# Performance work log

Hardware: AMD Instinct MI355X
Metric: run time of the kernel (lower is better)

The kernel has to match this reference:

```python
import jax, jax.numpy as jnp
import numpy as np

BG_W = 1.0
DILATED_BG_W = 5.0
EDGE_W = 20.0
KSIZE = 3


def setup_inputs() -> dict:
    key = jax.random.key(0)
    k1, k2 = jax.random.split(key)
    B, C, H, W = 16, 1, 1024, 1024
    pred = jax.random.normal(k1, (B, C, H, W), dtype=jnp.float32)
    target = (jax.random.uniform(k2, (B, C, H, W)) < 0.05).astype(jnp.float32)
    return {"pred": pred, "target": target}


def _dilate(target):
    # cv2.dilate with KSIZExKSIZE rect kernel == max pool, stride 1, SAME padding
    return jax.lax.reduce_window(
        target, -jnp.inf, jax.lax.max,
        window_dimensions=(1, 1, KSIZE, KSIZE),
        window_strides=(1, 1, 1, 1),
        padding="SAME",
    )


def reference(pred, target):
    dilated = _dilate(target)
    # weight: edge pixels (target>0.5) -> EDGE_W, else dilated band -> DILATED_BG_W, else BG_W
    weight = jnp.where(target > 0.5, EDGE_W,
                       jnp.where(dilated > 0.5, DILATED_BG_W, BG_W))
    # binary_cross_entropy_with_logits, reduction='none', then mean
    x = pred
    losses = weight * (jnp.maximum(x, 0.0) - x * target + jnp.log1p(jnp.exp(-jnp.abs(x))))
    return jnp.mean(losses)
```

## Files before the change

### kernel.cpp

```cpp
#include <hip/hip_runtime.h>

#define HH 1024
#define WW 1024
#define RPB 4
#define NT 1024

__device__ __forceinline__ float fmax3(float a, float b, float c) {
    return fmaxf(a, fmaxf(b, c));
}

__device__ __forceinline__ float loss_elem(float x, float t, float dil) {
    float w = fmaf(15.0f, t, fmaf(4.0f, dil, 1.0f));
    float a  = fabsf(x);
    float sp = __logf(1.0f + __expf(-a));
    return w * (fmaxf(x, 0.0f) - x * t + sp);
}

template <bool PER_WAVE>
__global__ __launch_bounds__(NT) void dilatedweightBCE_main(
        const float* __restrict__ pred,
        const float* __restrict__ target,
        float* __restrict__ partial) {
    __shared__ float swave[NT / 64];

    const int t    = threadIdx.x;
    const int lane = t & 63;
    const int w16  = t >> 6;
    const int rin  = t >> 8;
    const int c    = (t & 255) * 4;
    const int b    = blockIdx.y;
    const int h    = blockIdx.x * RPB + rin;

    const float* timg = target + (size_t)b * HH * WW;
    const size_t rowoff = (size_t)h * WW;
    const bool has_up = (h > 0);
    const bool has_dn = (h < HH - 1);
    const float4 zero = make_float4(0.0f, 0.0f, 0.0f, 0.0f);

    float4 tmid = *(const float4*)(timg + rowoff + c);
    float4 tup  = has_up ? *(const float4*)(timg + rowoff - WW + c) : zero;
    float4 tdn  = has_dn ? *(const float4*)(timg + rowoff + WW + c) : zero;
    float4 x    = *(const float4*)(pred + (size_t)b * HH * WW + rowoff + c);

    float halo = 0.0f;
    if (lane == 0 || lane == 63) {
        const int pc = (lane == 0) ? c - 1 : c + 4;
        if (pc >= 0 && pc < WW) {
            float v = timg[rowoff + pc];
            if (has_up) v = fmaxf(v, timg[rowoff - WW + pc]);
            if (has_dn) v = fmaxf(v, timg[rowoff + WW + pc]);
            halo = v;
        }
    }

    float4 vm = make_float4(fmax3(tup.x, tmid.x, tdn.x),
                            fmax3(tup.y, tmid.y, tdn.y),
                            fmax3(tup.z, tmid.z, tdn.z),
                            fmax3(tup.w, tmid.w, tdn.w));

    float l  = __shfl_up(vm.w, 1);
    float rr = __shfl_down(vm.x, 1);
    if (lane == 0)  l  = halo;
    if (lane == 63) rr = halo;

    float d0 = fmax3(l,    vm.x, vm.y);
    float d1 = fmax3(vm.x, vm.y, vm.z);
    float d2 = fmax3(vm.y, vm.z, vm.w);
    float d3 = fmax3(vm.z, vm.w, rr);

    float s = 0.0f;
    s += loss_elem(x.x, tmid.x, d0);
    s += loss_elem(x.y, tmid.y, d1);
    s += loss_elem(x.z, tmid.z, d2);
    s += loss_elem(x.w, tmid.w, d3);

    #pragma unroll
    for (int off = 32; off > 0; off >>= 1)
        s += __shfl_down(s, off);

    if (PER_WAVE) {
        if (lane == 0)
            partial[((size_t)blockIdx.y * gridDim.x + blockIdx.x) * (NT / 64) + w16] = s;
    } else {
        if (lane == 0) swave[w16] = s;
        __syncthreads();
        if (t < 64) {
            float v = (lane < NT / 64) ? swave[lane] : 0.0f;
            #pragma unroll
            for (int off = 8; off > 0; off >>= 1)
                v += __shfl_down(v, off);
            if (lane == 0)
                partial[(size_t)blockIdx.y * gridDim.x + blockIdx.x] = v;
        }
    }
}

__global__ __launch_bounds__(NT) void dilatedweightBCE_reduce(
        const float* __restrict__ partial,
        float* __restrict__ out,
        int npart4,
        float inv_n) {
    __shared__ float swave[NT / 64];
    const int t = threadIdx.x;

    float s = 0.0f;
    const float4* p4 = (const float4*)partial;
    for (int i = t; i < npart4; i += NT) {
        float4 v = p4[i];
        s += v.x + v.y + v.z + v.w;
    }

    #pragma unroll
    for (int off = 32; off > 0; off >>= 1)
        s += __shfl_down(s, off);

    const int lane = t & 63;
    if (lane == 0) swave[t >> 6] = s;
    __syncthreads();
    if (t == 0) {
        float tot = 0.0f;
        #pragma unroll
        for (int i = 0; i < NT / 64; ++i) tot += swave[i];
        out[0] = tot * inv_n;
    }
}

extern "C" void kernel_launch(void* const* d_in, const int* in_sizes, int n_in,
                              void* d_out, int out_size, void* d_ws, size_t ws_size,
                              hipStream_t stream) {
    const float* pred   = (const float*)d_in[0];
    const float* target = (const float*)d_in[1];
    float* out     = (float*)d_out;
    float* partial = (float*)d_ws;

    const int n  = in_sizes[0];
    const int Bn = n / (HH * WW);
    const int nblocks = (HH / RPB) * Bn;

    dim3 grid(HH / RPB, Bn);
    const size_t need = (size_t)nblocks * (NT / 64) * sizeof(float);
    if (ws_size >= need) {
        dilatedweightBCE_main<true><<<grid, NT, 0, stream>>>(pred, target, partial);
        dilatedweightBCE_reduce<<<1, NT, 0, stream>>>(partial, out,
                                                      nblocks * (NT / 64) / 4,
                                                      1.0f / (float)n);
    } else {
        dilatedweightBCE_main<false><<<grid, NT, 0, stream>>>(pred, target, partial);
        dilatedweightBCE_reduce<<<1, NT, 0, stream>>>(partial, out,
                                                      nblocks / 4, 1.0f / (float)n);
    }
}
```

Baseline: 158.8 us.

## Stage target row bands in LDS via direct global-to-LDS loads

Each block now handles an 8-row band with 512 threads. The target rows plus a one-row halo above and below go into LDS through global_load_lds, and each thread computes 4 rows from that staged data. This cuts the redundant target reads of the old scheme, which fetched every target row three times, down to a 10/8 overhead. The cost is 40KB of LDS per block, which lowers occupancy, and a block-wide barrier before compute.

```diff
diff --git a/kernel.cpp b/kernel.cpp
--- a/kernel.cpp
+++ b/kernel.cpp
@@ -2,8 +2,9 @@
 
 #define HH 1024
 #define WW 1024
-#define RPB 4
-#define NT 1024
+#define BAND 8
+#define NT 512
+#define LDSF ((BAND + 2) * WW)
 
 __device__ __forceinline__ float fmax3(float a, float b, float c) {
     return fmaxf(a, fmaxf(b, c));
@@ -16,96 +17,128 @@
     return w * (fmaxf(x, 0.0f) - x * t + sp);
 }
 
+__device__ __forceinline__ void load_to_lds16(const float* g, float* l) {
+    __builtin_amdgcn_global_load_lds(
+        (const __attribute__((address_space(1))) void*)g,
+        (__attribute__((address_space(3))) void*)l,
+        16, 0, 0);
+}
+
 template <bool PER_WAVE>
 __global__ __launch_bounds__(NT) void dilatedweightBCE_main(
         const float* __restrict__ pred,
         const float* __restrict__ target,
         float* __restrict__ partial) {
-    __shared__ float swave[NT / 64];
+    __shared__ float lds[LDSF];
 
     const int t    = threadIdx.x;
     const int lane = t & 63;
-    const int w16  = t >> 6;
-    const int rin  = t >> 8;
-    const int c    = (t & 255) * 4;
+    const int wv   = t >> 6;
     const int b    = blockIdx.y;
-    const int h    = blockIdx.x * RPB + rin;
+    const int h0   = blockIdx.x * BAND;
 
     const float* timg = target + (size_t)b * HH * WW;
-    const size_t rowoff = (size_t)h * WW;
-    const bool has_up = (h > 0);
-    const bool has_dn = (h < HH - 1);
-    const float4 zero = make_float4(0.0f, 0.0f, 0.0f, 0.0f);
+    const float* pimg = pred   + (size_t)b * HH * WW;
 
-    float4 tmid = *(const float4*)(timg + rowoff + c);
-    float4 tup  = has_up ? *(const float4*)(timg + rowoff - WW + c) : zero;
-    float4 tdn  = has_dn ? *(const float4*)(timg + rowoff + WW + c) : zero;
-    float4 x    = *(const float4*)(pred + (size_t)b * HH * WW + rowoff + c);
+    const float4 zero4 = make_float4(0.0f, 0.0f, 0.0f, 0.0f);
+    if (h0 == 0 && t < WW / 4) ((float4*)lds)[t] = zero4;
+    if (h0 + BAND == HH && t >= NT - WW / 4)
+        ((float4*)(lds + (BAND + 1) * WW))[t - (NT - WW / 4)] = zero4;
 
-    float halo = 0.0f;
+    const float* src = timg + (long long)(h0 - 1) * WW;
+    #pragma unroll
+    for (int k = 0; k < LDSF / (NT * 4); ++k) {
+        const int idx = k * NT + t;
+        const int r   = idx >> 8;
+        const bool valid = (h0 - 1 + r >= 0) && (h0 - 1 + r < HH);
+        if (valid) load_to_lds16(src + (size_t)idx * 4, lds + (size_t)idx * 4);
+    }
+
+    const int rg4 = (t >> 8) * 4;
+    const int c   = (t & 255) * 4;
+    float4 xr[4];
+    #pragma unroll
+    for (int j = 0; j < 4; ++j)
+        xr[j] = *(const float4*)(pimg + (size_t)(h0 + rg4 + j) * WW + c);
+
+    __syncthreads();
+
+    float halo[4];
+    #pragma unroll
+    for (int j = 0; j < 4; ++j) halo[j] = 0.0f;
     if (lane == 0 || lane == 63) {
         const int pc = (lane == 0) ? c - 1 : c + 4;
         if (pc >= 0 && pc < WW) {
-            float v = timg[rowoff + pc];
-            if (has_up) v = fmaxf(v, timg[rowoff - WW + pc]);
-            if (has_dn) v = fmaxf(v, timg[rowoff + WW + pc]);
-            halo = v;
+            float hv[6];
+            #pragma unroll
+            for (int i = 0; i < 6; ++i)
+                hv[i] = lds[(rg4 + i) * WW + pc];
+            #pragma unroll
+            for (int j = 0; j < 4; ++j)
+                halo[j] = fmax3(hv[j], hv[j + 1], hv[j + 2]);
         }
     }
 
-    float4 vm = make_float4(fmax3(tup.x, tmid.x, tdn.x),
-                            fmax3(tup.y, tmid.y, tdn.y),
-                            fmax3(tup.z, tmid.z, tdn.z),
-                            fmax3(tup.w, tmid.w, tdn.w));
-
-    float l  = __shfl_up(vm.w, 1);
-    float rr = __shfl_down(vm.x, 1);
-    if (lane == 0)  l  = halo;
-    if (lane == 63) rr = halo;
-
-    float d0 = fmax3(l,    vm.x, vm.y);
-    float d1 = fmax3(vm.x, vm.y, vm.z);
-    float d2 = fmax3(vm.y, vm.z, vm.w);
-    float d3 = fmax3(vm.z, vm.w, rr);
+    float4 R[6];
+    #pragma unroll
+    for (int i = 0; i < 6; ++i)
+        R[i] = *(const float4*)(lds + (rg4 + i) * WW + c);
 
     float s = 0.0f;
-    s += loss_elem(x.x, tmid.x, d0);
-    s += loss_elem(x.y, tmid.y, d1);
-    s += loss_elem(x.z, tmid.z, d2);
-    s += loss_elem(x.w, tmid.w, d3);
+    #pragma unroll
+    for (int j = 0; j < 4; ++j) {
+        float4 a = R[j], m = R[j + 1], d = R[j + 2];
+        float4 vm = make_float4(fmax3(a.x, m.x, d.x), fmax3(a.y, m.y, d.y),
+                                fmax3(a.z, m.z, d.z), fmax3(a.w, m.w, d.w));
+
+        float l  = __shfl_up(vm.w, 1);
+        float rr = __shfl_down(vm.x, 1);
+        if (lane == 0)  l  = halo[j];
+        if (lane == 63) rr = halo[j];
+
+        float d0 = fmax3(l,    vm.x, vm.y);
+        float d1 = fmax3(vm.x, vm.y, vm.z);
+        float d2 = fmax3(vm.y, vm.z, vm.w);
+        float d3 = fmax3(vm.z, vm.w, rr);
+
+        float4 x = xr[j];
+        s += loss_elem(x.x, m.x, d0);
+        s += loss_elem(x.y, m.y, d1);
+        s += loss_elem(x.z, m.z, d2);
+        s += loss_elem(x.w, m.w, d3);
+    }
 
     #pragma unroll
     for (int off = 32; off > 0; off >>= 1)
         s += __shfl_down(s, off);
 
+    const size_t bid = (size_t)blockIdx.y * gridDim.x + blockIdx.x;
     if (PER_WAVE) {
-        if (lane == 0)
-            partial[((size_t)blockIdx.y * gridDim.x + blockIdx.x) * (NT / 64) + w16] = s;
+        if (lane == 0) partial[bid * 8 + wv] = s;
     } else {
-        if (lane == 0) swave[w16] = s;
         __syncthreads();
-        if (t < 64) {
-            float v = (lane < NT / 64) ? swave[lane] : 0.0f;
+        if (lane == 0) lds[wv] = s;
+        __syncthreads();
+        if (t == 0) {
+            float tot = 0.0f;
             #pragma unroll
-            for (int off = 8; off > 0; off >>= 1)
-                v += __shfl_down(v, off);
-            if (lane == 0)
-                partial[(size_t)blockIdx.y * gridDim.x + blockIdx.x] = v;
+            for (int i = 0; i < 8; ++i) tot += lds[i];
+            partial[bid] = tot;
         }
     }
 }
 
-__global__ __launch_bounds__(NT) void dilatedweightBCE_reduce(
+__global__ __launch_bounds__(1024) void dilatedweightBCE_reduce(
         const float* __restrict__ partial,
         float* __restrict__ out,
         int npart4,
         float inv_n) {
-    __shared__ float swave[NT / 64];
+    __shared__ float swave[16];
     const int t = threadIdx.x;
 
     float s = 0.0f;
     const float4* p4 = (const float4*)partial;
-    for (int i = t; i < npart4; i += NT) {
+    for (int i = t; i < npart4; i += 1024) {
         float4 v = p4[i];
         s += v.x + v.y + v.z + v.w;
     }
@@ -120,7 +153,7 @@
     if (t == 0) {
         float tot = 0.0f;
         #pragma unroll
-        for (int i = 0; i < NT / 64; ++i) tot += swave[i];
+        for (int i = 0; i < 16; ++i) tot += swave[i];
         out[0] = tot * inv_n;
     }
 }
@@ -135,18 +168,19 @@
 
     const int n  = in_sizes[0];
     const int Bn = n / (HH * WW);
-    const int nblocks = (HH / RPB) * Bn;
+    const int nblocks = (HH / BAND) * Bn;
 
-    dim3 grid(HH / RPB, Bn);
-    const size_t need = (size_t)nblocks * (NT / 64) * sizeof(float);
+    dim3 grid(HH / BAND, Bn);
+    const size_t need = (size_t)nblocks * 8 * sizeof(float);
     if (ws_size >= need) {
         dilatedweightBCE_main<true><<<grid, NT, 0, stream>>>(pred, target, partial);
-        dilatedweightBCE_reduce<<<1, NT, 0, stream>>>(partial, out,
-                                                      nblocks * (NT / 64) / 4,
-                                                      1.0f / (float)n);
+        dilatedweightBCE_reduce<<<1, 1024, 0, stream>>>(partial, out,
+                                                        nblocks * 8 / 4,
+                                                        1.0f / (float)n);
     } else {
         dilatedweightBCE_main<false><<<grid, NT, 0, stream>>>(pred, target, partial);
-        dilatedweightBCE_reduce<<<1, NT, 0, stream>>>(partial, out,
-                                                      nblocks / 4, 1.0f / (float)n);
+        dilatedweightBCE_reduce<<<1, 1024, 0, stream>>>(partial, out,
+                                                        nblocks / 4,
+                                                        1.0f / (float)n);
     }
 }
```

Result: faster. 146.3 us (-7.9%).
